# Kernel optimization log

Measured on AMD Instinct MI355X. Metric: run time of the kernel, lower is better.

Reference implementation:

```python
import jax, jax.numpy as jnp
import numpy as np

N, E, B = 50000, 500000, 64
IN_DIM, HID, H, NC = 128, 32, 8, 10
SLOPE = 0.2  # DGL GATConv leaky_relu negative_slope default


def setup_inputs() -> dict:
    key = jax.random.key(0)
    ks = jax.random.split(key, 14)
    feat = jax.random.normal(ks[0], (N, IN_DIM), dtype=jnp.float32)
    src = jax.random.randint(ks[1], (E,), 0, N, dtype=jnp.int32)
    dst = jax.random.randint(ks[2], (E,), 0, N, dtype=jnp.int32)
    node2graph = jnp.sort(jax.random.randint(ks[3], (N,), 0, B, dtype=jnp.int32))
    s1 = 1.0 / np.sqrt(IN_DIM)
    s2 = 1.0 / np.sqrt(H * HID)
    W1 = jax.random.normal(ks[4], (IN_DIM, H * HID), dtype=jnp.float32) * s1
    al1 = jax.random.normal(ks[5], (H, HID), dtype=jnp.float32) * 0.1
    ar1 = jax.random.normal(ks[6], (H, HID), dtype=jnp.float32) * 0.1
    b1 = jnp.zeros((H * HID,), dtype=jnp.float32)
    W2 = jax.random.normal(ks[7], (H * HID, H * HID), dtype=jnp.float32) * s2
    al2 = jax.random.normal(ks[8], (H, HID), dtype=jnp.float32) * 0.1
    ar2 = jax.random.normal(ks[9], (H, HID), dtype=jnp.float32) * 0.1
    b2 = jnp.zeros((H * HID,), dtype=jnp.float32)
    Wc = jax.random.normal(ks[10], (H * HID, NC), dtype=jnp.float32) * s2
    bc = jnp.zeros((NC,), dtype=jnp.float32)
    return dict(feat=feat, src=src, dst=dst, node2graph=node2graph,
                W1=W1, al1=al1, ar1=ar1, b1=b1,
                W2=W2, al2=al2, ar2=ar2, b2=b2, Wc=Wc, bc=bc)


def gat_layer(h, src, dst, W, al, ar, b):
    # h: [N, F_in] -> out: [N, H, HID]   (DGL GATConv math, no dropout)
    fs = (h @ W).reshape(N, H, HID)                      # projected src/dst feats
    el = jnp.sum(fs * al[None], axis=-1)                 # [N, H]
    er = jnp.sum(fs * ar[None], axis=-1)                 # [N, H]
    e = jax.nn.leaky_relu(el[src] + er[dst], SLOPE)      # [E, H] per-edge logits
    # edge softmax over incoming edges of each dst node (numerically stable)
    emax = jax.ops.segment_max(e, dst, num_segments=N)   # [N, H]
    ex = jnp.exp(e - emax[dst])                          # [E, H]
    denom = jax.ops.segment_sum(ex, dst, num_segments=N) # [N, H]
    alpha = ex / denom[dst]                              # [E, H]
    msg = alpha[:, :, None] * fs[src]                    # [E, H, HID]
    rst = jax.ops.segment_sum(msg, dst, num_segments=N)  # [N, H, HID]
    return rst + b.reshape(1, H, HID)


def reference(feat, src, dst, node2graph, W1, al1, ar1, b1, W2, al2, ar2, b2, Wc, bc):
    h = jax.nn.relu(gat_layer(feat, src, dst, W1, al1, ar1, b1)).reshape(N, H * HID)
    h = gat_layer(h, src, dst, W2, al2, ar2, b2).reshape(N, H * HID)
    # dgl.mean_nodes: per-graph mean over nodes of the batched graph
    counts = jax.ops.segment_sum(jnp.ones((N,), dtype=h.dtype), node2graph, num_segments=B)
    hg = jax.ops.segment_sum(h, node2graph, num_segments=B) / jnp.maximum(counts, 1.0)[:, None]
    return hg @ Wc + bc  # [B, NC]
```

## Files before the change

kernel.cpp:

```cpp
#include <hip/hip_runtime.h>
#include <hip/hip_bf16.h>

#define N_NODES 50000
#define N_EDGES 500000
#define N_GRAPHS 64
#define FDIM 256
#define NHEAD 8
#define NC 10
#define SLOPE 0.2f
#define MPAD 50048
#define NBKT 196
#define CNTN (NBKT * 256)
#define SCAN_NB (CNTN / 1024)
#define NB1 256
#define EPB 1956
#define LDSW 40
#define PSPLIT 16
#define CAST_THREADS (256*128 + 256*256 + N_NODES)
#define CAST_NB ((CAST_THREADS + 255) / 256)

typedef __attribute__((ext_vector_type(8))) short bf16x8;
typedef __attribute__((ext_vector_type(4))) float f32x4;
typedef __attribute__((ext_vector_type(2))) float f32x2;
typedef __attribute__((ext_vector_type(4))) unsigned u32x4;

__device__ __forceinline__ unsigned short f2bf(float f) {
  unsigned x = __float_as_uint(f);
  x += 0x7fff + ((x >> 16) & 1);
  return (unsigned short)(x >> 16);
}
__device__ __forceinline__ float b2f(unsigned short u) {
  return __uint_as_float((unsigned)u << 16);
}
__device__ __forceinline__ int fswz(int node, int off) {
  return off ^ ((node & 7) << 5) ^ (((node >> 3) & 1) << 4);
}

__global__ void cast_hist_kernel(const float* __restrict__ W1, const float* __restrict__ W2,
                                 unsigned short* __restrict__ Wt1, unsigned short* __restrict__ Wt2,
                                 const int* __restrict__ n2g, int* __restrict__ gstart,
                                 const int* __restrict__ dst, int* __restrict__ counts,
                                 int* __restrict__ rowstart) {
  int t = threadIdx.x;
  if (blockIdx.x < NB1) {
    __shared__ int hist[NBKT];
    int b = blockIdx.x;
    if (t < NBKT) hist[t] = 0;
    __syncthreads();
    int start = b * EPB;
    int end = min(start + EPB, N_EDGES);
    for (int base = start + t * 4; base < end; base += 1024) {
      if (base + 3 < end) {
        int4 d = *(const int4*)(dst + base);
        atomicAdd(&hist[d.x >> 8], 1); atomicAdd(&hist[d.y >> 8], 1);
        atomicAdd(&hist[d.z >> 8], 1); atomicAdd(&hist[d.w >> 8], 1);
      } else {
        for (int e2 = base; e2 < end; ++e2) atomicAdd(&hist[dst[e2] >> 8], 1);
      }
    }
    __syncthreads();
    if (t < NBKT) counts[t * NB1 + b] = hist[t];
    return;
  }
  int e = (blockIdx.x - NB1) * 256 + t;
  if (e == 0) rowstart[N_NODES] = N_EDGES;
  if (e < 256 * 128) {
    int n = e / 128, k = e % 128;
    Wt1[(size_t)n * 128 + k] = f2bf(W1[(size_t)k * 256 + n]);
  } else if (e < 256 * 128 + 256 * 256) {
    int t2 = e - 256 * 128;
    int n = t2 / 256, k = t2 % 256;
    Wt2[(size_t)n * 256 + k] = f2bf(W2[(size_t)k * 256 + n]);
  } else {
    int i = e - (256 * 128 + 256 * 256);
    if (i < N_NODES) {
      int g1 = n2g[i];
      int g0 = (i == 0) ? -1 : n2g[i - 1];
      for (int g = g0 + 1; g <= g1; ++g) gstart[g] = i;
      if (i == N_NODES - 1) {
        for (int g = g1 + 1; g <= N_GRAPHS; ++g) gstart[g] = N_NODES;
      }
    }
  }
}

__global__ void scan_local_kernel(const int* __restrict__ deg, int* __restrict__ outv,
                                  int* __restrict__ bsum, int n) {
  __shared__ int ws[4];
  int t = threadIdx.x, lane = t & 63, w = t >> 6;
  int base = blockIdx.x * 1024 + t * 4;
  int4 v = make_int4(0, 0, 0, 0);
  if (base + 3 < n) {
    v = *(const int4*)(deg + base);
  } else {
    if (base + 0 < n) v.x = deg[base + 0];
    if (base + 1 < n) v.y = deg[base + 1];
    if (base + 2 < n) v.z = deg[base + 2];
    if (base + 3 < n) v.w = deg[base + 3];
  }
  int s = v.x + v.y + v.z + v.w;
  int x = s;
  #pragma unroll
  for (int off = 1; off < 64; off <<= 1) {
    int y = __shfl_up(x, off);
    if (lane >= off) x += y;
  }
  if (lane == 63) ws[w] = x;
  __syncthreads();
  int woff = 0;
  #pragma unroll
  for (int i = 0; i < 4; ++i) woff += (i < w) ? ws[i] : 0;
  int excl = woff + x - s;
  int4 o;
  o.x = excl;
  o.y = excl + v.x;
  o.z = excl + v.x + v.y;
  o.w = excl + v.x + v.y + v.z;
  if (base + 3 < n) {
    *(int4*)(outv + base) = o;
  } else {
    if (base + 0 < n) outv[base + 0] = o.x;
    if (base + 1 < n) outv[base + 1] = o.y;
    if (base + 2 < n) outv[base + 2] = o.z;
    if (base + 3 < n) outv[base + 3] = o.w;
  }
  if (t == 255) bsum[blockIdx.x] = woff + x;
}

__global__ void bucket_scatter_kernel(const int* __restrict__ src, const int* __restrict__ dst,
                                      const int* __restrict__ cbase, const int* __restrict__ bsum,
                                      int2* __restrict__ ebuf) {
  __shared__ int cur[NBKT];
  __shared__ int boffl[SCAN_NB];
  int t = threadIdx.x, b = blockIdx.x;
  if (t < 64) {
    int v = (t < SCAN_NB) ? bsum[t] : 0;
    int x = v;
    #pragma unroll
    for (int off = 1; off < 64; off <<= 1) {
      int y = __shfl_up(x, off);
      if (t >= off) x += y;
    }
    if (t < SCAN_NB) boffl[t] = x - v;
  }
  __syncthreads();
  if (t < NBKT) {
    int idx = t * NB1 + b;
    cur[t] = cbase[idx] + boffl[idx >> 10];
  }
  __syncthreads();
  int start = b * EPB;
  int end = min(start + EPB, N_EDGES);
  for (int base = start + t * 4; base < end; base += 1024) {
    if (base + 3 < end) {
      int4 s = *(const int4*)(src + base);
      int4 d = *(const int4*)(dst + base);
      int r;
      r = atomicAdd(&cur[d.x >> 8], 1); ebuf[r] = make_int2(s.x, d.x);
      r = atomicAdd(&cur[d.y >> 8], 1); ebuf[r] = make_int2(s.y, d.y);
      r = atomicAdd(&cur[d.z >> 8], 1); ebuf[r] = make_int2(s.z, d.z);
      r = atomicAdd(&cur[d.w >> 8], 1); ebuf[r] = make_int2(s.w, d.w);
    } else {
      for (int e2 = base; e2 < end; ++e2) {
        int dd = dst[e2];
        int r = atomicAdd(&cur[dd >> 8], 1);
        ebuf[r] = make_int2(src[e2], dd);
      }
    }
  }
}

__global__ void csr_bucket_kernel(const int2* __restrict__ ebuf, const int* __restrict__ cbase,
                                  const int* __restrict__ bsum,
                                  int* __restrict__ rowstart, int* __restrict__ esrc) {
  __shared__ int hist[256];
  __shared__ int cur[256];
  __shared__ int ws[4];
  __shared__ int boffl[SCAN_NB];
  int t = threadIdx.x;
  int bkt = blockIdx.x;
  hist[t] = 0;
  if (t >= 64 && t < 128) {
    int tt = t - 64;
    int v = (tt < SCAN_NB) ? bsum[tt] : 0;
    int x = v;
    #pragma unroll
    for (int off = 1; off < 64; off <<= 1) {
      int y = __shfl_up(x, off);
      if (tt >= off) x += y;
    }
    if (tt < SCAN_NB) boffl[tt] = x - v;
  }
  __syncthreads();
  int i0 = bkt * NB1;
  int segstart = cbase[i0] + boffl[i0 >> 10];
  int segend = N_EDGES;
  if (bkt + 1 < NBKT) {
    int i1 = (bkt + 1) * NB1;
    segend = cbase[i1] + boffl[i1 >> 10];
  }
  for (int e = segstart + t; e < segend; e += 256)
    atomicAdd(&hist[ebuf[e].y & 255], 1);
  __syncthreads();
  int lane = t & 63, w = t >> 6;
  int v = hist[t], x = v;
  #pragma unroll
  for (int off = 1; off < 64; off <<= 1) {
    int y = __shfl_up(x, off);
    if (lane >= off) x += y;
  }
  if (lane == 63) ws[w] = x;
  __syncthreads();
  int woff = 0;
  #pragma unroll
  for (int i = 0; i < 4; ++i) woff += (i < w) ? ws[i] : 0;
  int excl = woff + x - v;
  cur[t] = excl;
  int node = bkt * 256 + t;
  if (node < N_NODES) rowstart[node] = segstart + excl;
  __syncthreads();
  for (int e = segstart + t; e < segend; e += 256) {
    int2 p = ebuf[e];
    int r = atomicAdd(&cur[p.y & 255], 1);
    esrc[segstart + r] = p.x;
  }
}

template<int K, bool AF32>
__global__ void gemm_mfma(const void* __restrict__ Avoid,
                          const unsigned short* __restrict__ Wt,
                          unsigned char* __restrict__ fs,
                          const float* __restrict__ al, const float* __restrict__ ar,
                          float* __restrict__ el, float* __restrict__ er, int nrows) {
  constexpr int KC = K / 32;
  __shared__ __align__(16) unsigned short LDSbuf[(64 + 256) * LDSW];
  unsigned short* Albs = LDSbuf;
  unsigned short* Wlds = LDSbuf + 64 * LDSW;
  const float* Af = (const float*)Avoid;
  const unsigned short* Ab = (const unsigned short*)Avoid;
  int t = threadIdx.x;
  int lane = t & 63;
  int w = t >> 6;
  int row0 = blockIdx.x * 64;
  int m = lane & 15;
  int q = lane >> 4;
  float4 a32[2];
  bf16x8 a16;
  bf16x8 wtr[4];
  int arow = t >> 2, apiece = t & 3;
  int agrow = min(row0 + arow, nrows - 1);
  int frow0 = t >> 3, fquad0 = t & 7;
  int frow1 = (256 + t) >> 3, fquad1 = t & 7;
  int fgrow0 = min(row0 + frow0, nrows - 1);
  int fgrow1 = min(row0 + frow1, nrows - 1);

  auto stage = [&](int kc) {
    if (AF32) {
      a32[0] = *(const float4*)(Af + (size_t)fgrow0 * K + kc * 32 + fquad0 * 4);
      a32[1] = *(const float4*)(Af + (size_t)fgrow1 * K + kc * 32 + fquad1 * 4);
    } else {
      a16 = *(const bf16x8*)(Ab + (size_t)agrow * K + kc * 32 + apiece * 8);
    }
    #pragma unroll
    for (int j = 0; j < 4; ++j) {
      int row = j * 64 + (t >> 2);
      wtr[j] = *(const bf16x8*)(Wt + (size_t)row * K + kc * 32 + (t & 3) * 8);
    }
  };
  auto commit = [&]() {
    if (AF32) {
      ushort4 o0, o1;
      o0.x = f2bf(a32[0].x); o0.y = f2bf(a32[0].y); o0.z = f2bf(a32[0].z); o0.w = f2bf(a32[0].w);
      o1.x = f2bf(a32[1].x); o1.y = f2bf(a32[1].y); o1.z = f2bf(a32[1].z); o1.w = f2bf(a32[1].w);
      *(ushort4*)(Albs + frow0 * LDSW + fquad0 * 4) = o0;
      *(ushort4*)(Albs + frow1 * LDSW + fquad1 * 4) = o1;
    } else {
      *(bf16x8*)(Albs + arow * LDSW + apiece * 8) = a16;
    }
    #pragma unroll
    for (int j = 0; j < 4; ++j) {
      int row = j * 64 + (t >> 2);
      *(bf16x8*)(Wlds + row * LDSW + (t & 3) * 8) = wtr[j];
    }
  };

  f32x4 acc[16];
  #pragma unroll
  for (int nt = 0; nt < 16; ++nt) acc[nt] = (f32x4){0.f, 0.f, 0.f, 0.f};

  stage(0);
  commit();
  for (int kc = 0; kc < KC; ++kc) {
    __syncthreads();
    if (kc + 1 < KC) stage(kc + 1);
    bf16x8 af = *(const bf16x8*)(Albs + (w * 16 + m) * LDSW + q * 8);
    #pragma unroll
    for (int nt = 0; nt < 16; ++nt) {
      bf16x8 bfv = *(const bf16x8*)(Wlds + (nt * 16 + m) * LDSW + q * 8);
      acc[nt] = __builtin_amdgcn_mfma_f32_16x16x32_bf16(bfv, af, acc[nt], 0, 0, 0);
    }
    __syncthreads();
    if (kc + 1 < KC) commit();
  }
  unsigned char* fsst = (unsigned char*)LDSbuf;
  float* elst = (float*)(fsst + 16384);
  float* erst = elst + 512;

  int nloc = w * 16 + m;
  float elh[NHEAD], erh[NHEAD];
  #pragma unroll
  for (int h = 0; h < NHEAD; ++h) { elh[h] = 0.f; erh[h] = 0.f; }
  #pragma unroll
  for (int nt = 0; nt < 16; ++nt) {
    int h = nt >> 1;
    int c0 = (nt & 1) * 16 + q * 4;
    float4 a4 = *(const float4*)(al + h * 32 + c0);
    float4 r4 = *(const float4*)(ar + h * 32 + c0);
    elh[h] += acc[nt][0] * a4.x + acc[nt][1] * a4.y + acc[nt][2] * a4.z + acc[nt][3] * a4.w;
    erh[h] += acc[nt][0] * r4.x + acc[nt][1] * r4.y + acc[nt][2] * r4.z + acc[nt][3] * r4.w;
  }
  #pragma unroll
  for (int h = 0; h < NHEAD; ++h) {
    elh[h] += __shfl_xor(elh[h], 16); elh[h] += __shfl_xor(elh[h], 32);
    erh[h] += __shfl_xor(erh[h], 16); erh[h] += __shfl_xor(erh[h], 32);
  }
  #pragma unroll
  for (int nt = 0; nt < 16; ++nt) {
    int pk = 0;
    pk = __builtin_amdgcn_cvt_pk_fp8_f32(acc[nt][0], acc[nt][1], pk, false);
    pk = __builtin_amdgcn_cvt_pk_fp8_f32(acc[nt][2], acc[nt][3], pk, true);
    *(unsigned*)(fsst + nloc * 256 + fswz(nloc, nt * 16 + q * 4)) = (unsigned)pk;
  }
  *(float2*)(elst + nloc * 8 + q * 2) = make_float2(elh[2 * q], elh[2 * q + 1]);
  *(float2*)(erst + nloc * 8 + q * 2) = make_float2(erh[2 * q], erh[2 * q + 1]);
  __syncthreads();
  #pragma unroll
  for (int i = 0; i < 4; ++i) {
    int p = i * 4096 + t * 16;
    int nn = p >> 8, off = p & 255;
    u32x4 d = *(const u32x4*)(fsst + nn * 256 + fswz(nn, off));
    *(u32x4*)(fs + (size_t)row0 * 256 + p) = d;
  }
  if (t < 128) {
    *(float4*)(el + (size_t)row0 * 8 + t * 4) = *(const float4*)(elst + t * 4);
  } else {
    int tt = t - 128;
    *(float4*)(er + (size_t)row0 * 8 + tt * 4) = *(const float4*)(erst + tt * 4);
  }
}

template<bool RELU>
__global__ __launch_bounds__(256, 6)
void edge_agg_kernel(const int* __restrict__ rowstart, const int* __restrict__ esrc,
                     const float* __restrict__ el, const float* __restrict__ er,
                     const unsigned char* __restrict__ fs,
                     const float* __restrict__ bias,
                     unsigned short* __restrict__ out, int nnodes) {
  int lane = threadIdx.x & 63;
  int w = threadIdx.x >> 6;
  int v0 = (blockIdx.x * 4 + w) * 4;
  if (v0 >= nnodes) return;
  int h = lane >> 3;
  int t8 = lane >> 3;
  int hh = lane & 7;
  const unsigned char* fsl = fs + lane * 4;
  const float* elp = el;
  const float4 b = *(const float4*)(bias + lane * 4);

  int rsl = rowstart[min(v0 + lane, nnodes)];
  int rs[5];
  #pragma unroll
  for (int i = 0; i < 5; ++i) rs[i] = __shfl(rsl, i);
  int degv[4], mmx[4], es[4];
  float erw[4];
  #pragma unroll
  for (int i = 0; i < 4; ++i) {
    degv[i] = rs[i + 1] - rs[i];
    mmx[i] = min(degv[i], 64);
    erw[i] = er[(unsigned)(v0 + i) * 8u + hh];
    es[i] = 0;
    if (mmx[i] > 0) es[i] = esrc[rs[i] + min(lane, mmx[i] - 1)];
  }

  auto issue = [&](int esv, int mmv, float erv, int gbase, float& x, unsigned* f) {
    int sj = __shfl(esv, max(min(gbase + t8, mmv - 1), 0));
    x = elp[(unsigned)sj * 8u + hh] + erv;
    #pragma unroll
    for (int t = 0; t < 8; ++t) {
      int s = __shfl(esv, max(min(gbase + t, mmv - 1), 0));
      f[t] = *(const unsigned*)(fsl + ((unsigned)s << 8));
    }
  };

  float xC; unsigned fC[8];
  issue(es[0], mmx[0], erw[0], 0, xC, fC);

  #pragma unroll
  for (int i = 0; i < 4; ++i) {
    float4 acc0 = make_float4(0.f, 0.f, 0.f, 0.f);
    float4 acc1 = make_float4(0.f, 0.f, 0.f, 0.f);
    float ws0 = 0.f, ws1 = 0.f;
    int G = max((mmx[i] + 7) >> 3, 1);
    for (int g = 0; g < G; ++g) {
      bool last = (g + 1 >= G);
      float xN = 0.f; unsigned fN[8];
      #pragma unroll
      for (int t = 0; t < 8; ++t) fN[t] = 0u;
      if (!(last && i == 3)) {
        int esn = last ? es[(i < 3) ? i + 1 : 3] : es[i];
        int mmn = last ? mmx[(i < 3) ? i + 1 : 3] : mmx[i];
        float ern = last ? erw[(i < 3) ? i + 1 : 3] : erw[i];
        int gbn = last ? 0 : (g + 1) * 8;
        issue(esn, mmn, ern, gbn, xN, fN);
      }
      float xl = fmaxf(xC, SLOPE * xC);
      float wp = __expf(xl);
      if (g * 8 + t8 >= mmx[i]) wp = 0.f;
      float wt[8];
      #pragma unroll
      for (int t = 0; t < 8; ++t) wt[t] = __shfl(wp, t * 8 + h);
      #pragma unroll
      for (int t = 0; t < 8; ++t) {
        float wgt = wt[t];
        f32x2 lo = __builtin_amdgcn_cvt_pk_f32_fp8(fC[t], false);
        f32x2 hi = __builtin_amdgcn_cvt_pk_f32_fp8(fC[t], true);
        if (t & 1) {
          ws1 += wgt;
          acc1.x = fmaf(wgt, lo.x, acc1.x);
          acc1.y = fmaf(wgt, lo.y, acc1.y);
          acc1.z = fmaf(wgt, hi.x, acc1.z);
          acc1.w = fmaf(wgt, hi.y, acc1.w);
        } else {
          ws0 += wgt;
          acc0.x = fmaf(wgt, lo.x, acc0.x);
          acc0.y = fmaf(wgt, lo.y, acc0.y);
          acc0.z = fmaf(wgt, hi.x, acc0.z);
          acc0.w = fmaf(wgt, hi.y, acc0.w);
        }
      }
      xC = xN;
      #pragma unroll
      for (int t = 0; t < 8; ++t) fC[t] = fN[t];
    }
    if (__builtin_expect(degv[i] > 64, 0)) {
      for (int base = 64; base < degv[i]; base += 64) {
        int mm2 = min(degv[i] - base, 64);
        int es2 = esrc[rs[i] + base + min(lane, mm2 - 1)];
        for (int j0 = 0; j0 < mm2; j0 += 8) {
          int sj = __shfl(es2, min(j0 + t8, mm2 - 1));
          float x = elp[(unsigned)sj * 8u + hh] + erw[i];
          x = fmaxf(x, SLOPE * x);
          float wp2 = __expf(x);
          if (j0 + t8 >= mm2) wp2 = 0.f;
          float wt[8]; unsigned f2[8];
          #pragma unroll
          for (int t = 0; t < 8; ++t) wt[t] = __shfl(wp2, t * 8 + h);
          #pragma unroll
          for (int t = 0; t < 8; ++t) {
            int s = __shfl(es2, min(j0 + t, mm2 - 1));
            f2[t] = *(const unsigned*)(fsl + ((unsigned)s << 8));
          }
          #pragma unroll
          for (int t = 0; t < 8; ++t) {
            float wgt = wt[t];
            f32x2 lo = __builtin_amdgcn_cvt_pk_f32_fp8(f2[t], false);
            f32x2 hi = __builtin_amdgcn_cvt_pk_f32_fp8(f2[t], true);
            if (t & 1) {
              ws1 += wgt;
              acc1.x = fmaf(wgt, lo.x, acc1.x); acc1.y = fmaf(wgt, lo.y, acc1.y);
              acc1.z = fmaf(wgt, hi.x, acc1.z); acc1.w = fmaf(wgt, hi.y, acc1.w);
            } else {
              ws0 += wgt;
              acc0.x = fmaf(wgt, lo.x, acc0.x); acc0.y = fmaf(wgt, lo.y, acc0.y);
              acc0.z = fmaf(wgt, hi.x, acc0.z); acc0.w = fmaf(wgt, hi.y, acc0.w);
            }
          }
        }
      }
    }
    float wsum = ws0 + ws1;
    float4 acc;
    acc.x = acc0.x + acc1.x; acc.y = acc0.y + acc1.y;
    acc.z = acc0.z + acc1.z; acc.w = acc0.w + acc1.w;
    float rdenom = (degv[i] > 0) ? (1.0f / wsum) : 0.f;
    acc.x = fmaf(acc.x, rdenom, b.x);
    acc.y = fmaf(acc.y, rdenom, b.y);
    acc.z = fmaf(acc.z, rdenom, b.z);
    acc.w = fmaf(acc.w, rdenom, b.w);
    if (RELU) {
      acc.x = fmaxf(acc.x, 0.f); acc.y = fmaxf(acc.y, 0.f);
      acc.z = fmaxf(acc.z, 0.f); acc.w = fmaxf(acc.w, 0.f);
    }
    ushort4 o;
    o.x = f2bf(acc.x); o.y = f2bf(acc.y); o.z = f2bf(acc.z); o.w = f2bf(acc.w);
    *(ushort4*)(out + (size_t)(v0 + i) * FDIM + lane * 4) = o;
  }
}

__global__ void pool_partial_kernel(const unsigned short* __restrict__ h2,
                                    const int* __restrict__ gstart,
                                    float* __restrict__ ppart) {
  int t = threadIdx.x;
  int g = blockIdx.x / PSPLIT;
  int s = blockIdx.x % PSPLIT;
  int n0 = gstart[g], n1 = gstart[g + 1];
  int cnt = n1 - n0;
  int chunk = (cnt + PSPLIT - 1) / PSPLIT;
  int a = n0 + s * chunk;
  int bnd = min(a + chunk, n1);
  float s0 = 0.f, s1 = 0.f, s2 = 0.f, s3 = 0.f;
  int n = a;
  for (; n + 4 <= bnd; n += 4) {
    s0 += b2f(h2[(size_t)(n + 0) * FDIM + t]);
    s1 += b2f(h2[(size_t)(n + 1) * FDIM + t]);
    s2 += b2f(h2[(size_t)(n + 2) * FDIM + t]);
    s3 += b2f(h2[(size_t)(n + 3) * FDIM + t]);
  }
  for (; n < bnd; ++n) s0 += b2f(h2[(size_t)n * FDIM + t]);
  ppart[(size_t)blockIdx.x * FDIM + t] = (s0 + s1) + (s2 + s3);
}

__global__ void pool_cls_kernel(const float* __restrict__ ppart, const int* __restrict__ gstart,
                                const float* __restrict__ Wc, const float* __restrict__ bcv,
                                float* __restrict__ out) {
  __shared__ float hgl[FDIM];
  int t = threadIdx.x, g = blockIdx.x;
  float s = 0.f;
  #pragma unroll
  for (int sp = 0; sp < PSPLIT; ++sp)
    s += ppart[(size_t)(g * PSPLIT + sp) * FDIM + t];
  hgl[t] = s;
  __syncthreads();
  int cnt = gstart[g + 1] - gstart[g];
  float inv = (cnt > 0) ? (1.0f / (float)cnt) : 1.0f;
  int w = t >> 6, lane = t & 63;
  for (int j = w; j < NC; j += 4) {
    float p = 0.f;
    #pragma unroll
    for (int k = 0; k < 4; ++k) {
      int c = lane * 4 + k;
      p += hgl[c] * Wc[c * NC + j];
    }
    #pragma unroll
    for (int off = 1; off < 64; off <<= 1) p += __shfl_xor(p, off);
    if (lane == 0) out[g * NC + j] = p * inv + bcv[j];
  }
}

extern "C" void kernel_launch(void* const* d_in, const int* in_sizes, int n_in,
                              void* d_out, int out_size, void* d_ws, size_t ws_size,
                              hipStream_t stream) {
  const float* feat = (const float*)d_in[0];
  const int* src    = (const int*)d_in[1];
  const int* dst    = (const int*)d_in[2];
  const int* n2g    = (const int*)d_in[3];
  const float* W1  = (const float*)d_in[4];
  const float* al1 = (const float*)d_in[5];
  const float* ar1 = (const float*)d_in[6];
  const float* b1  = (const float*)d_in[7];
  const float* W2  = (const float*)d_in[8];
  const float* al2 = (const float*)d_in[9];
  const float* ar2 = (const float*)d_in[10];
  const float* b2  = (const float*)d_in[11];
  const float* Wc  = (const float*)d_in[12];
  const float* bc  = (const float*)d_in[13];
  float* out = (float*)d_out;

  char* wp = (char*)d_ws;
  auto carve = [&](size_t bytes) -> void* {
    void* p = (void*)wp;
    wp += (bytes + 255) & ~(size_t)255;
    return p;
  };
  unsigned char* fs = (unsigned char*)carve((size_t)MPAD * FDIM);
  unsigned short* h1 = (unsigned short*)carve((size_t)MPAD * FDIM * 2);
  unsigned short* h2 = h1;
  unsigned short* Wt1 = (unsigned short*)carve((size_t)256 * 128 * 2);
  unsigned short* Wt2 = (unsigned short*)carve((size_t)256 * 256 * 2);
  float* el      = (float*)carve((size_t)MPAD * NHEAD * 4);
  float* er      = (float*)carve((size_t)MPAD * NHEAD * 4);
  int* rowstart  = (int*)  carve((size_t)(N_NODES + 1) * 4);
  int* esrc      = (int*)  carve((size_t)N_EDGES * 4);
  int* gstart    = (int*)  carve((size_t)(N_GRAPHS + 1) * 4);
  int* bsum      = (int*)  carve((size_t)SCAN_NB * 4);
  int* counts    = (int*)  carve((size_t)CNTN * 4);
  int* cbase     = (int*)  carve((size_t)CNTN * 4);
  int2* ebuf     = (int2*) carve((size_t)N_EDGES * 8);
  float* ppart   = (float*)carve((size_t)N_GRAPHS * PSPLIT * FDIM * 4);
  (void)ws_size; (void)n_in; (void)in_sizes; (void)out_size;

  cast_hist_kernel<<<NB1 + CAST_NB, 256, 0, stream>>>(
      W1, W2, Wt1, Wt2, n2g, gstart, dst, counts, rowstart);
  scan_local_kernel<<<SCAN_NB, 256, 0, stream>>>(counts, cbase, bsum, CNTN);
  bucket_scatter_kernel<<<NB1, 256, 0, stream>>>(src, dst, cbase, bsum, ebuf);
  csr_bucket_kernel<<<NBKT, 256, 0, stream>>>(ebuf, cbase, bsum, rowstart, esrc);

  gemm_mfma<128, true><<<MPAD / 64, 256, 0, stream>>>(
      (const void*)feat, Wt1, fs, al1, ar1, el, er, N_NODES);
  edge_agg_kernel<true><<<(N_NODES + 15) / 16, 256, 0, stream>>>(
      rowstart, esrc, el, er, fs, b1, h1, N_NODES);

  gemm_mfma<256, false><<<MPAD / 64, 256, 0, stream>>>(
      (const void*)h1, Wt2, fs, al2, ar2, el, er, N_NODES);
  edge_agg_kernel<false><<<(N_NODES + 15) / 16, 256, 0, stream>>>(
      rowstart, esrc, el, er, fs, b2, h2, N_NODES);

  pool_partial_kernel<<<N_GRAPHS * PSPLIT, 256, 0, stream>>>(h2, gstart, ppart);
  pool_cls_kernel<<<N_GRAPHS, 256, 0, stream>>>(ppart, gstart, Wc, bc, out);
}
```

Measured before the change: 254.7 us.

## Assign one node per wavefront in edge aggregation, dropping cross-node prefetch

Restructures the edge aggregation kernel so each wavefront handles a single destination node instead of four, with a simple loop over 8-edge groups plus a masked tail. The software prefetch that overlapped the next group's gathers with current compute is removed, and the launch bound goes from 6 to 8 waves. The aim is to cut register pressure and raise occupancy so hardware multithreading hides gather latency. The trade-off is losing explicit load/compute overlap and the per-wave amortization of rowstart reads.

```diff
diff --git a/kernel.cpp b/kernel.cpp
--- a/kernel.cpp
+++ b/kernel.cpp
@@ -350,80 +350,50 @@
 }
 
 template<bool RELU>
-__global__ __launch_bounds__(256, 6)
+__global__ __launch_bounds__(256, 8)
 void edge_agg_kernel(const int* __restrict__ rowstart, const int* __restrict__ esrc,
                      const float* __restrict__ el, const float* __restrict__ er,
                      const unsigned char* __restrict__ fs,
                      const float* __restrict__ bias,
                      unsigned short* __restrict__ out, int nnodes) {
+  int gid = blockIdx.x * blockDim.x + threadIdx.x;
+  int v = gid >> 6;
   int lane = threadIdx.x & 63;
-  int w = threadIdx.x >> 6;
-  int v0 = (blockIdx.x * 4 + w) * 4;
-  if (v0 >= nnodes) return;
+  if (v >= nnodes) return;
   int h = lane >> 3;
   int t8 = lane >> 3;
   int hh = lane & 7;
+  int row0 = rowstart[v];
+  int deg = rowstart[v + 1] - row0;
+  float er_w = er[v * NHEAD + hh];
   const unsigned char* fsl = fs + lane * 4;
   const float* elp = el;
-  const float4 b = *(const float4*)(bias + lane * 4);
-
-  int rsl = rowstart[min(v0 + lane, nnodes)];
-  int rs[5];
-  #pragma unroll
-  for (int i = 0; i < 5; ++i) rs[i] = __shfl(rsl, i);
-  int degv[4], mmx[4], es[4];
-  float erw[4];
-  #pragma unroll
-  for (int i = 0; i < 4; ++i) {
-    degv[i] = rs[i + 1] - rs[i];
-    mmx[i] = min(degv[i], 64);
-    erw[i] = er[(unsigned)(v0 + i) * 8u + hh];
-    es[i] = 0;
-    if (mmx[i] > 0) es[i] = esrc[rs[i] + min(lane, mmx[i] - 1)];
-  }
-
-  auto issue = [&](int esv, int mmv, float erv, int gbase, float& x, unsigned* f) {
-    int sj = __shfl(esv, max(min(gbase + t8, mmv - 1), 0));
-    x = elp[(unsigned)sj * 8u + hh] + erv;
-    #pragma unroll
-    for (int t = 0; t < 8; ++t) {
-      int s = __shfl(esv, max(min(gbase + t, mmv - 1), 0));
-      f[t] = *(const unsigned*)(fsl + ((unsigned)s << 8));
-    }
-  };
-
-  float xC; unsigned fC[8];
-  issue(es[0], mmx[0], erw[0], 0, xC, fC);
-
-  #pragma unroll
-  for (int i = 0; i < 4; ++i) {
-    float4 acc0 = make_float4(0.f, 0.f, 0.f, 0.f);
-    float4 acc1 = make_float4(0.f, 0.f, 0.f, 0.f);
-    float ws0 = 0.f, ws1 = 0.f;
-    int G = max((mmx[i] + 7) >> 3, 1);
-    for (int g = 0; g < G; ++g) {
-      bool last = (g + 1 >= G);
-      float xN = 0.f; unsigned fN[8];
+  float4 acc0 = make_float4(0.f, 0.f, 0.f, 0.f);
+  float4 acc1 = make_float4(0.f, 0.f, 0.f, 0.f);
+  float ws0 = 0.f, ws1 = 0.f;
+
+  for (int base = 0; base < deg; base += 64) {
+    int mm = min(deg - base, 64);
+    int es = esrc[row0 + base + min(lane, mm - 1)];
+    int full = mm & ~7;
+    for (int j0 = 0; j0 < full; j0 += 8) {
+      int sj = __shfl(es, j0 + t8);
+      float x = elp[(unsigned)sj * 8u + hh] + er_w;
+      x = fmaxf(x, SLOPE * x);
+      float wp = __expf(x);
+      float wt[8]; unsigned f[8];
       #pragma unroll
-      for (int t = 0; t < 8; ++t) fN[t] = 0u;
-      if (!(last && i == 3)) {
-        int esn = last ? es[(i < 3) ? i + 1 : 3] : es[i];
-        int mmn = last ? mmx[(i < 3) ? i + 1 : 3] : mmx[i];
-        float ern = last ? erw[(i < 3) ? i + 1 : 3] : erw[i];
-        int gbn = last ? 0 : (g + 1) * 8;
-        issue(esn, mmn, ern, gbn, xN, fN);
-      }
-      float xl = fmaxf(xC, SLOPE * xC);
-      float wp = __expf(xl);
-      if (g * 8 + t8 >= mmx[i]) wp = 0.f;
-      float wt[8];
+      for (int t = 0; t < 8; ++t) {
+        int s = __shfl(es, j0 + t);
+        f[t] = *(const unsigned*)(fsl + ((unsigned)s << 8));
+      }
       #pragma unroll
       for (int t = 0; t < 8; ++t) wt[t] = __shfl(wp, t * 8 + h);
       #pragma unroll
       for (int t = 0; t < 8; ++t) {
         float wgt = wt[t];
-        f32x2 lo = __builtin_amdgcn_cvt_pk_f32_fp8(fC[t], false);
-        f32x2 hi = __builtin_amdgcn_cvt_pk_f32_fp8(fC[t], true);
+        f32x2 lo = __builtin_amdgcn_cvt_pk_f32_fp8(f[t], false);
+        f32x2 hi = __builtin_amdgcn_cvt_pk_f32_fp8(f[t], true);
         if (t & 1) {
           ws1 += wgt;
           acc1.x = fmaf(wgt, lo.x, acc1.x);
@@ -438,63 +408,59 @@
           acc0.w = fmaf(wgt, hi.y, acc0.w);
         }
       }
-      xC = xN;
+    }
+    if (full < mm) {
+      int sj = __shfl(es, min(full + t8, mm - 1));
+      float x = elp[(unsigned)sj * 8u + hh] + er_w;
+      x = fmaxf(x, SLOPE * x);
+      float wp = __expf(x);
+      if (full + t8 >= mm) wp = 0.f;
+      float wt[8]; unsigned f[8];
       #pragma unroll
-      for (int t = 0; t < 8; ++t) fC[t] = fN[t];
-    }
-    if (__builtin_expect(degv[i] > 64, 0)) {
-      for (int base = 64; base < degv[i]; base += 64) {
-        int mm2 = min(degv[i] - base, 64);
-        int es2 = esrc[rs[i] + base + min(lane, mm2 - 1)];
-        for (int j0 = 0; j0 < mm2; j0 += 8) {
-          int sj = __shfl(es2, min(j0 + t8, mm2 - 1));
-          float x = elp[(unsigned)sj * 8u + hh] + erw[i];
-          x = fmaxf(x, SLOPE * x);
-          float wp2 = __expf(x);
-          if (j0 + t8 >= mm2) wp2 = 0.f;
-          float wt[8]; unsigned f2[8];
-          #pragma unroll
-          for (int t = 0; t < 8; ++t) wt[t] = __shfl(wp2, t * 8 + h);
-          #pragma unroll
-          for (int t = 0; t < 8; ++t) {
-            int s = __shfl(es2, min(j0 + t, mm2 - 1));
-            f2[t] = *(const unsigned*)(fsl + ((unsigned)s << 8));
-          }
-          #pragma unroll
-          for (int t = 0; t < 8; ++t) {
-            float wgt = wt[t];
-            f32x2 lo = __builtin_amdgcn_cvt_pk_f32_fp8(f2[t], false);
-            f32x2 hi = __builtin_amdgcn_cvt_pk_f32_fp8(f2[t], true);
-            if (t & 1) {
-              ws1 += wgt;
-              acc1.x = fmaf(wgt, lo.x, acc1.x); acc1.y = fmaf(wgt, lo.y, acc1.y);
-              acc1.z = fmaf(wgt, hi.x, acc1.z); acc1.w = fmaf(wgt, hi.y, acc1.w);
-            } else {
-              ws0 += wgt;
-              acc0.x = fmaf(wgt, lo.x, acc0.x); acc0.y = fmaf(wgt, lo.y, acc0.y);
-              acc0.z = fmaf(wgt, hi.x, acc0.z); acc0.w = fmaf(wgt, hi.y, acc0.w);
-            }
-          }
+      for (int t = 0; t < 8; ++t) {
+        int s = __shfl(es, min(full + t, mm - 1));
+        f[t] = *(const unsigned*)(fsl + ((unsigned)s << 8));
+      }
+      #pragma unroll
+      for (int t = 0; t < 8; ++t) wt[t] = __shfl(wp, t * 8 + h);
+      #pragma unroll
+      for (int t = 0; t < 8; ++t) {
+        float wgt = wt[t];
+        f32x2 lo = __builtin_amdgcn_cvt_pk_f32_fp8(f[t], false);
+        f32x2 hi = __builtin_amdgcn_cvt_pk_f32_fp8(f[t], true);
+        if (t & 1) {
+          ws1 += wgt;
+          acc1.x = fmaf(wgt, lo.x, acc1.x);
+          acc1.y = fmaf(wgt, lo.y, acc1.y);
+          acc1.z = fmaf(wgt, hi.x, acc1.z);
+          acc1.w = fmaf(wgt, hi.y, acc1.w);
+        } else {
+          ws0 += wgt;
+          acc0.x = fmaf(wgt, lo.x, acc0.x);
+          acc0.y = fmaf(wgt, lo.y, acc0.y);
+          acc0.z = fmaf(wgt, hi.x, acc0.z);
+          acc0.w = fmaf(wgt, hi.y, acc0.w);
         }
       }
     }
-    float wsum = ws0 + ws1;
-    float4 acc;
-    acc.x = acc0.x + acc1.x; acc.y = acc0.y + acc1.y;
-    acc.z = acc0.z + acc1.z; acc.w = acc0.w + acc1.w;
-    float rdenom = (degv[i] > 0) ? (1.0f / wsum) : 0.f;
-    acc.x = fmaf(acc.x, rdenom, b.x);
-    acc.y = fmaf(acc.y, rdenom, b.y);
-    acc.z = fmaf(acc.z, rdenom, b.z);
-    acc.w = fmaf(acc.w, rdenom, b.w);
-    if (RELU) {
-      acc.x = fmaxf(acc.x, 0.f); acc.y = fmaxf(acc.y, 0.f);
-      acc.z = fmaxf(acc.z, 0.f); acc.w = fmaxf(acc.w, 0.f);
-    }
-    ushort4 o;
-    o.x = f2bf(acc.x); o.y = f2bf(acc.y); o.z = f2bf(acc.z); o.w = f2bf(acc.w);
-    *(ushort4*)(out + (size_t)(v0 + i) * FDIM + lane * 4) = o;
-  }
+  }
+  float wsum = ws0 + ws1;
+  float4 acc;
+  acc.x = acc0.x + acc1.x; acc.y = acc0.y + acc1.y;
+  acc.z = acc0.z + acc1.z; acc.w = acc0.w + acc1.w;
+  float rdenom = (deg > 0) ? (1.0f / wsum) : 0.f;
+  const float4 b = *(const float4*)(bias + lane * 4);
+  acc.x = fmaf(acc.x, rdenom, b.x);
+  acc.y = fmaf(acc.y, rdenom, b.y);
+  acc.z = fmaf(acc.z, rdenom, b.z);
+  acc.w = fmaf(acc.w, rdenom, b.w);
+  if (RELU) {
+    acc.x = fmaxf(acc.x, 0.f); acc.y = fmaxf(acc.y, 0.f);
+    acc.z = fmaxf(acc.z, 0.f); acc.w = fmaxf(acc.w, 0.f);
+  }
+  ushort4 o;
+  o.x = f2bf(acc.x); o.y = f2bf(acc.y); o.z = f2bf(acc.z); o.w = f2bf(acc.w);
+  *(ushort4*)(out + (size_t)v * FDIM + lane * 4) = o;
 }
 
 __global__ void pool_partial_kernel(const unsigned short* __restrict__ h2,
@@ -597,12 +563,12 @@
 
   gemm_mfma<128, true><<<MPAD / 64, 256, 0, stream>>>(
       (const void*)feat, Wt1, fs, al1, ar1, el, er, N_NODES);
-  edge_agg_kernel<true><<<(N_NODES + 15) / 16, 256, 0, stream>>>(
+  edge_agg_kernel<true><<<(N_NODES * 64 + 255) / 256, 256, 0, stream>>>(
       rowstart, esrc, el, er, fs, b1, h1, N_NODES);
 
   gemm_mfma<256, false><<<MPAD / 64, 256, 0, stream>>>(
       (const void*)h1, Wt2, fs, al2, ar2, el, er, N_NODES);
-  edge_agg_kernel<false><<<(N_NODES + 15) / 16, 256, 0, stream>>>(
+  edge_agg_kernel<false><<<(N_NODES * 64 + 255) / 256, 256, 0, stream>>>(
       rowstart, esrc, el, er, fs, b2, h2, N_NODES);
 
   pool_partial_kernel<<<N_GRAPHS * PSPLIT, 256, 0, stream>>>(h2, gstart, ppart);
```

Result: faster. 214.3 us (-15.9%).
